# Optimization experiments

Hardware: AMD Instinct MI355X
Metric: run time of the kernel (lower is better)

Reference implementation:

```python
import jax, jax.numpy as jnp
import numpy as np

EPS = 1e-5

def conv2d(x, w, padding):
    # x: (N, Cin, H, W), w: (Cout, Cin, kh, kw)
    return jax.lax.conv_general_dilated(
        x, w, window_strides=(1, 1),
        padding=[(padding, padding), (padding, padding)],
        dimension_numbers=('NCHW', 'OIHW', 'NCHW'))

def proj_bn_relu(x, w, gamma, beta, mean, var):
    # 1x1 conv + BatchNorm (eval mode, running stats) + ReLU
    y = conv2d(x, w, 0)
    scale = (gamma / jnp.sqrt(var + EPS))[None, :, None, None]
    shift = (beta - mean * gamma / jnp.sqrt(var + EPS))[None, :, None, None]
    return jax.nn.relu(y * scale + shift)

def setup_inputs() -> dict:
    key = jax.random.key(0)
    ks = jax.random.split(key, 16)
    B, Sx, Sy, C1, C2, Co, H, W, K = 2, 4, 4, 64, 64, 64, 128, 128, 3
    inp = {
        'u': jax.random.normal(ks[0], (B, Sx, C1, H, W), jnp.float32),
        'v': jax.random.normal(ks[1], (B, Sy, C2, H, W), jnp.float32),
        'pu_w': jax.random.normal(ks[2], (C1, C1, 1, 1), jnp.float32) * 0.05,
        'pu_gamma': jnp.ones((C1,), jnp.float32),
        'pu_beta': jnp.zeros((C1,), jnp.float32),
        'pu_mean': jax.random.normal(ks[3], (C1,), jnp.float32) * 0.1,
        'pu_var': jax.random.uniform(ks[4], (C1,), jnp.float32, 0.5, 1.5),
        'pv_w': jax.random.normal(ks[5], (C2, C2, 1, 1), jnp.float32) * 0.05,
        'pv_gamma': jnp.ones((C2,), jnp.float32),
        'pv_beta': jnp.zeros((C2,), jnp.float32),
        'pv_mean': jax.random.normal(ks[6], (C2,), jnp.float32) * 0.1,
        'pv_var': jax.random.uniform(ks[7], (C2,), jnp.float32, 0.5, 1.5),
        'conv_w': jax.random.normal(ks[8], (Co, C1 + C2, K, K), jnp.float32) * 0.02,
        'conv_b': jax.random.normal(ks[9], (Co,), jnp.float32) * 0.02,
    }
    return inp

def reference(u, v, pu_w, pu_gamma, pu_beta, pu_mean, pu_var,
              pv_w, pv_gamma, pv_beta, pv_mean, pv_var, conv_w, conv_b):
    B, Sx, C1, H, W = u.shape
    _, Sy, C2, _, _ = v.shape
    pad = 1
    # flatten set dims into batch for the 1x1 proj+BN+ReLU
    uf = proj_bn_relu(u.reshape(B * Sx, C1, H, W), pu_w, pu_gamma, pu_beta, pu_mean, pu_var)
    vf = proj_bn_relu(v.reshape(B * Sy, C2, H, W), pv_w, pv_gamma, pv_beta, pv_mean, pv_var)
    # conv over concat channels is linear -> split weight and broadcast-add,
    # exactly equal to conv(cat(repeat(u), repeat(v))) without materializing
    # the (B,Sx,Sy,C1+C2,H,W) tensor.
    w_u = conv_w[:, :C1]   # (Co, C1, K, K)
    w_v = conv_w[:, C1:]   # (Co, C2, K, K)
    ou = conv2d(uf, w_u, pad)  # (B*Sx, Co, Ho, Wo)
    ov = conv2d(vf, w_v, pad)  # (B*Sy, Co, Ho, Wo)
    Co, Ho, Wo = ou.shape[1], ou.shape[2], ou.shape[3]
    ou = ou.reshape(B, Sx, 1, Co, Ho, Wo)
    ov = ov.reshape(B, 1, Sy, Co, Ho, Wo)
    out = ou + ov + conv_b[None, None, None, :, None, None]
    return out  # (B, Sx, Sy, Co, Ho, Wo)
```

## Files before the change

kernel.cpp:

```cpp
#include <hip/hip_runtime.h>
#include <hip/hip_bf16.h>

#define C   64
#define Hh  128
#define Ww  128
#define HW  16384

typedef __attribute__((ext_vector_type(8))) short bf16x8;
typedef __attribute__((ext_vector_type(4))) float f32x4;

__device__ __forceinline__ unsigned short f2bf(float f) {
    unsigned u = __builtin_bit_cast(unsigned, f);
    unsigned r = (u + 0x7fff + ((u >> 16) & 1)) >> 16;
    return (unsigned short)r;
}

__global__ __launch_bounds__(256) void prep_kernel(
    const float* __restrict__ pu_w, const float* __restrict__ pu_g,
    const float* __restrict__ pu_b, const float* __restrict__ pu_m,
    const float* __restrict__ pu_v,
    const float* __restrict__ pv_w, const float* __restrict__ pv_g,
    const float* __restrict__ pv_b, const float* __restrict__ pv_m,
    const float* __restrict__ pv_v,
    const float* __restrict__ conv_w,
    short* __restrict__ pwu, short* __restrict__ pwv,
    short* __restrict__ wpu, short* __restrict__ wpv,
    float* __restrict__ shu, float* __restrict__ shv)
{
    const int idx = blockIdx.x * 256 + threadIdx.x;
    if (idx < 8192) {
        const int c  = idx >> 12;
        const int r  = idx & 4095;
        const int co = r >> 6, ci = r & 63;
        const float* w = c ? pv_w : pu_w;
        const float* g = c ? pv_g : pu_g;
        const float* vv = c ? pv_v : pu_v;
        const float scale = g[co] * rsqrtf(vv[co] + 1e-5f);
        (c ? pwv : pwu)[r] = (short)f2bf(w[co * 64 + ci] * scale);
    } else if (idx < 81920) {
        const int flat = idx - 8192;
        const int c  = flat / 36864;
        const int r  = flat % 36864;
        const int ch  = r / 18432;
        const int r2  = r % 18432;
        const int tap = r2 / 2048;
        const int r3  = r2 & 2047;
        const int co = r3 >> 5, ci = r3 & 31;
        const float src = conv_w[(size_t)(co * 128 + c * 64 + ch * 32 + ci) * 9 + tap];
        (c ? wpv : wpu)[((ch * 9 + tap) * 64 + co) * 32 + ci] = (short)f2bf(src);
    } else if (idx < 82048) {
        const int r  = idx - 81920;
        const int c  = r >> 6, co = r & 63;
        const float* g = c ? pv_g : pu_g;
        const float* b = c ? pv_b : pu_b;
        const float* m = c ? pv_m : pu_m;
        const float* vv = c ? pv_v : pu_v;
        const float scale = g[co] * rsqrtf(vv[co] + 1e-5f);
        (c ? shv : shu)[co] = b[co] - m[co] * scale;
    }
}

__global__ __launch_bounds__(256) void proj_mfma(
    const float* __restrict__ x, const short* __restrict__ pw,
    const float* __restrict__ shiftg, short* __restrict__ y)
{
    __shared__ short xs[256 * 72];
    __shared__ short pwl[64 * 72];
    __shared__ float ssh[64];

    const int img  = blockIdx.y;
    const int pix0 = blockIdx.x * 256;
    const int tid  = threadIdx.x;

    const float* xi = x + (size_t)img * C * HW + pix0 + tid;
#pragma unroll 8
    for (int c2 = 0; c2 < 32; ++c2) {
        const float a = xi[(size_t)(2 * c2) * HW];
        const float b = xi[(size_t)(2 * c2 + 1) * HW];
        const int packed = (int)f2bf(a) | ((int)f2bf(b) << 16);
        *(int*)(&xs[tid * 72 + c2 * 2]) = packed;
    }
#pragma unroll
    for (int it = 0; it < 2; ++it) {
        const int idx = tid + it * 256;
        const int oct = idx & 7, co = idx >> 3;
        *(int4*)(&pwl[co * 72 + oct * 8]) = *(const int4*)(&pw[co * 64 + oct * 8]);
    }
    if (tid < 64) ssh[tid] = shiftg[tid];
    __syncthreads();

    const int wq = tid >> 6;
    const int lane = tid & 63;
    const int lx = lane & 15;
    const int q  = lane >> 4;

    f32x4 acc[4][4];
#pragma unroll
    for (int mt = 0; mt < 4; ++mt)
#pragma unroll
        for (int nt = 0; nt < 4; ++nt) acc[mt][nt] = (f32x4){0.f, 0.f, 0.f, 0.f};

#pragma unroll
    for (int kc = 0; kc < 2; ++kc) {
        bf16x8 a[4], b[4];
#pragma unroll
        for (int mt = 0; mt < 4; ++mt)
            a[mt] = *(const bf16x8*)&xs[((wq * 4 + mt) * 16 + lx) * 72 + kc * 32 + q * 8];
#pragma unroll
        for (int nt = 0; nt < 4; ++nt)
            b[nt] = *(const bf16x8*)&pwl[(nt * 16 + lx) * 72 + kc * 32 + q * 8];
#pragma unroll
        for (int mt = 0; mt < 4; ++mt)
#pragma unroll
            for (int nt = 0; nt < 4; ++nt)
                acc[mt][nt] = __builtin_amdgcn_mfma_f32_16x16x32_bf16(a[mt], b[nt], acc[mt][nt], 0, 0, 0);
    }

    short* yo = y + ((size_t)img * HW + pix0) * C;
#pragma unroll
    for (int mt = 0; mt < 4; ++mt)
#pragma unroll
        for (int nt = 0; nt < 4; ++nt)
#pragma unroll
            for (int r = 0; r < 4; ++r) {
                const int pixl = (wq * 4 + mt) * 16 + q * 4 + r;
                const int co = nt * 16 + lx;
                float vv = acc[mt][nt][r] + ssh[co];
                vv = fmaxf(vv, 0.f);
                yo[(size_t)pixl * C + co] = (short)f2bf(vv);
            }
}

__global__ __launch_bounds__(256, 2) void conv_mfma(
    const short* __restrict__ uf, const short* __restrict__ wp,
    float* __restrict__ out)
{
    __shared__ short xs[340 * 40];
    __shared__ short wsm[5 * 64 * 40];

    const int img = blockIdx.y;
    const int tx = blockIdx.x & 3, ty = blockIdx.x >> 2;
    const int h0 = ty * 8, w0 = tx * 32;
    const int tid = threadIdx.x;
    const int wq = tid >> 6;
    const int lane = tid & 63;
    const int lx = lane & 15;
    const int q8 = (lane >> 4) * 8;

    f32x4 acc[4][4];
#pragma unroll
    for (int mt = 0; mt < 4; ++mt)
#pragma unroll
        for (int nt = 0; nt < 4; ++nt) acc[mt][nt] = (f32x4){0.f, 0.f, 0.f, 0.f};

    const short* ub = uf + (size_t)img * HW * C;

    for (int ch = 0; ch < 2; ++ch) {
        __syncthreads();
        for (int idx = tid; idx < 1360; idx += 256) {
            const int oct = idx & 3;
            const int pcell = idx >> 2;
            const int h = pcell / 34, w = pcell - h * 34;
            const int gh = h0 - 1 + h, gw = w0 - 1 + w;
            int4 v = {0, 0, 0, 0};
            if (gh >= 0 && gh < Hh && gw >= 0 && gw < Ww)
                v = *(const int4*)&ub[(size_t)(gh * Ww + gw) * C + ch * 32 + oct * 8];
            *(int4*)(&xs[pcell * 40 + oct * 8]) = v;
        }
        for (int tg = 0; tg < 2; ++tg) {
            const int tb = tg ? 5 : 0;
            const int ntap = tg ? 4 : 5;
            if (tg) __syncthreads();
            for (int idx = tid; idx < ntap * 256; idx += 256) {
                const int oct = idx & 3;
                const int co = (idx >> 2) & 63;
                const int tl = idx >> 8;
                *(int4*)(&wsm[(tl * 64 + co) * 40 + oct * 8]) =
                    *(const int4*)&wp[(((ch * 9 + tb + tl) * 64) + co) * 32 + oct * 8];
            }
            __syncthreads();
            for (int tl = 0; tl < ntap; ++tl) {
                const int t = tb + tl;
                const int ky = (t < 3) ? 0 : ((t < 6) ? 1 : 2);
                const int kx = t - ky * 3;
                bf16x8 a[4], b[4];
#pragma unroll
                for (int mt = 0; mt < 4; ++mt)
                    a[mt] = *(const bf16x8*)&wsm[(tl * 64 + mt * 16 + lx) * 40 + q8];
#pragma unroll
                for (int nt = 0; nt < 4; ++nt) {
                    const int cell = (2 * wq + (nt >> 1) + ky) * 34 + (nt & 1) * 16 + lx + kx;
                    b[nt] = *(const bf16x8*)&xs[cell * 40 + q8];
                }
#pragma unroll
                for (int mt = 0; mt < 4; ++mt)
#pragma unroll
                    for (int nt = 0; nt < 4; ++nt)
                        acc[mt][nt] = __builtin_amdgcn_mfma_f32_16x16x32_bf16(a[mt], b[nt], acc[mt][nt], 0, 0, 0);
            }
        }
    }

    const int qq = lane >> 4;
    float* ob = out + (size_t)img * C * HW;
#pragma unroll
    for (int mt = 0; mt < 4; ++mt)
#pragma unroll
        for (int nt = 0; nt < 4; ++nt)
#pragma unroll
            for (int r = 0; r < 4; ++r) {
                const int co = mt * 16 + qq * 4 + r;
                const int h = h0 + 2 * wq + (nt >> 1);
                const int w = w0 + (nt & 1) * 16 + lx;
                ob[(size_t)co * HW + h * Ww + w] = acc[mt][nt][r];
            }
}

__global__ __launch_bounds__(256) void addb_kernel(
    const float* __restrict__ ou, const float* __restrict__ ov,
    const float* __restrict__ bias, float* __restrict__ out)
{
    const size_t i4 = (size_t)blockIdx.x * 256 + threadIdx.x;
    const int    hw4 = (int)(i4 & 4095);
    const size_t q   = i4 >> 12;
    const int co = (int)(q & 63);
    const size_t p = q >> 6;
    const int sy = (int)(p & 3);
    const int sx = (int)((p >> 2) & 3);
    const int b  = (int)(p >> 4);

    const float4 o1 = ((const float4*)ou)[((size_t)(b * 4 + sx) * C + co) * 4096 + hw4];
    const float4 o2 = ((const float4*)ov)[((size_t)(b * 4 + sy) * C + co) * 4096 + hw4];
    const float bb = bias[co];
    float4 r;
    r.x = o1.x + o2.x + bb;
    r.y = o1.y + o2.y + bb;
    r.z = o1.z + o2.z + bb;
    r.w = o1.w + o2.w + bb;
    ((float4*)out)[i4] = r;
}

extern "C" void kernel_launch(void* const* d_in, const int* in_sizes, int n_in,
                              void* d_out, int out_size, void* d_ws, size_t ws_size,
                              hipStream_t stream)
{
    const float* u        = (const float*)d_in[0];
    const float* v        = (const float*)d_in[1];
    const float* pu_w     = (const float*)d_in[2];
    const float* pu_gamma = (const float*)d_in[3];
    const float* pu_beta  = (const float*)d_in[4];
    const float* pu_mean  = (const float*)d_in[5];
    const float* pu_var   = (const float*)d_in[6];
    const float* pv_w     = (const float*)d_in[7];
    const float* pv_gamma = (const float*)d_in[8];
    const float* pv_beta  = (const float*)d_in[9];
    const float* pv_mean  = (const float*)d_in[10];
    const float* pv_var   = (const float*)d_in[11];
    const float* conv_w   = (const float*)d_in[12];
    const float* conv_b   = (const float*)d_in[13];
    float* out = (float*)d_out;

    char* ws = (char*)d_ws;
    short* uf  = (short*)(ws);
    short* vf  = (short*)(ws + 16777216);
    float* ou  = (float*)(ws + 33554432);
    float* ov  = (float*)(ws + 67108864);
    char*  aux = ws + 100663296;
    short* pwu = (short*)(aux);
    short* pwv = (short*)(aux + 8192);
    short* wpu = (short*)(aux + 16384);
    short* wpv = (short*)(aux + 90112);
    float* shu = (float*)(aux + 163840);
    float* shv = (float*)(aux + 164096);

    prep_kernel<<<321, 256, 0, stream>>>(pu_w, pu_gamma, pu_beta, pu_mean, pu_var,
                                         pv_w, pv_gamma, pv_beta, pv_mean, pv_var,
                                         conv_w, pwu, pwv, wpu, wpv, shu, shv);

    dim3 gp(64, 8);
    proj_mfma<<<gp, 256, 0, stream>>>(u, pwu, shu, uf);
    proj_mfma<<<gp, 256, 0, stream>>>(v, pwv, shv, vf);

    dim3 gc(64, 8);
    conv_mfma<<<gc, 256, 0, stream>>>(uf, wpu, ou);
    conv_mfma<<<gc, 256, 0, stream>>>(vf, wpv, ov);

    const size_t n4 = (size_t)out_size / 4;
    addb_kernel<<<(unsigned)(n4 / 256), 256, 0, stream>>>(ou, ov, conv_b, out);
}
```

Measured before the change: 279.8 us.

## Fuse 1x1 projection into 3x3 conv kernel and store conv outputs as bf16

Merges the projection+BN+ReLU step into the conv kernel. Each block converts the fp32 input tile plus its halo to bf16 in LDS, runs the 1x1 projection with MFMA in place, then runs the 3x3 conv from the same LDS tile. This removes the intermediate bf16 feature-map round trip and two launches, and u and v are handled in one launch via blockIdx.z. The conv partial outputs are now written as bf16 rather than fp32, halving their traffic into the broadcast-add kernel, which now reads 8 bf16 values per thread. In exchange, halo pixels are projected redundantly and the intermediate conv results lose precision.

```diff
diff --git a/kernel.cpp b/kernel.cpp
--- a/kernel.cpp
+++ b/kernel.cpp
@@ -13,6 +13,10 @@
     unsigned u = __builtin_bit_cast(unsigned, f);
     unsigned r = (u + 0x7fff + ((u >> 16) & 1)) >> 16;
     return (unsigned short)r;
+}
+__device__ __forceinline__ float bf2f(unsigned short h) {
+    unsigned u = ((unsigned)h) << 16;
+    return __builtin_bit_cast(float, u);
 }
 
 __global__ __launch_bounds__(256) void prep_kernel(
@@ -31,11 +35,12 @@
     if (idx < 8192) {
         const int c  = idx >> 12;
         const int r  = idx & 4095;
-        const int co = r >> 6, ci = r & 63;
+        const int co = r >> 6;
         const float* w = c ? pv_w : pu_w;
         const float* g = c ? pv_g : pu_g;
         const float* vv = c ? pv_v : pu_v;
         const float scale = g[co] * rsqrtf(vv[co] + 1e-5f);
+        const int ci = r & 63;
         (c ? pwv : pwu)[r] = (short)f2bf(w[co * 64 + ci] * scale);
     } else if (idx < 81920) {
         const int flat = idx - 8192;
@@ -60,92 +65,94 @@
     }
 }
 
-__global__ __launch_bounds__(256) void proj_mfma(
-    const float* __restrict__ x, const short* __restrict__ pw,
-    const float* __restrict__ shiftg, short* __restrict__ y)
-{
-    __shared__ short xs[256 * 72];
-    __shared__ short pwl[64 * 72];
+__global__ __launch_bounds__(256, 2) void fused_kernel(
+    const float* __restrict__ ug, const float* __restrict__ vg,
+    const short* __restrict__ pwu, const short* __restrict__ pwv,
+    const float* __restrict__ shu, const float* __restrict__ shv,
+    const short* __restrict__ wpu, const short* __restrict__ wpv,
+    short* __restrict__ oug, short* __restrict__ ovg)
+{
+    __shared__ short xs[352 * 72];
+    __shared__ short wbuf[3 * 64 * 40];
     __shared__ float ssh[64];
 
+    const int isv = blockIdx.z;
+    const float* x  = isv ? vg  : ug;
+    const short* pw = isv ? pwv : pwu;
+    const float* sh = isv ? shv : shu;
+    const short* wp = isv ? wpv : wpu;
+    short*       ot = isv ? ovg : oug;
+
     const int img  = blockIdx.y;
-    const int pix0 = blockIdx.x * 256;
-    const int tid  = threadIdx.x;
-
-    const float* xi = x + (size_t)img * C * HW + pix0 + tid;
-#pragma unroll 8
-    for (int c2 = 0; c2 < 32; ++c2) {
-        const float a = xi[(size_t)(2 * c2) * HW];
-        const float b = xi[(size_t)(2 * c2 + 1) * HW];
-        const int packed = (int)f2bf(a) | ((int)f2bf(b) << 16);
-        *(int*)(&xs[tid * 72 + c2 * 2]) = packed;
-    }
-#pragma unroll
-    for (int it = 0; it < 2; ++it) {
-        const int idx = tid + it * 256;
-        const int oct = idx & 7, co = idx >> 3;
-        *(int4*)(&pwl[co * 72 + oct * 8]) = *(const int4*)(&pw[co * 64 + oct * 8]);
-    }
-    if (tid < 64) ssh[tid] = shiftg[tid];
-    __syncthreads();
-
-    const int wq = tid >> 6;
-    const int lane = tid & 63;
-    const int lx = lane & 15;
-    const int q  = lane >> 4;
-
-    f32x4 acc[4][4];
-#pragma unroll
-    for (int mt = 0; mt < 4; ++mt)
-#pragma unroll
-        for (int nt = 0; nt < 4; ++nt) acc[mt][nt] = (f32x4){0.f, 0.f, 0.f, 0.f};
-
-#pragma unroll
-    for (int kc = 0; kc < 2; ++kc) {
-        bf16x8 a[4], b[4];
-#pragma unroll
-        for (int mt = 0; mt < 4; ++mt)
-            a[mt] = *(const bf16x8*)&xs[((wq * 4 + mt) * 16 + lx) * 72 + kc * 32 + q * 8];
-#pragma unroll
-        for (int nt = 0; nt < 4; ++nt)
-            b[nt] = *(const bf16x8*)&pwl[(nt * 16 + lx) * 72 + kc * 32 + q * 8];
-#pragma unroll
-        for (int mt = 0; mt < 4; ++mt)
-#pragma unroll
-            for (int nt = 0; nt < 4; ++nt)
-                acc[mt][nt] = __builtin_amdgcn_mfma_f32_16x16x32_bf16(a[mt], b[nt], acc[mt][nt], 0, 0, 0);
-    }
-
-    short* yo = y + ((size_t)img * HW + pix0) * C;
-#pragma unroll
-    for (int mt = 0; mt < 4; ++mt)
-#pragma unroll
-        for (int nt = 0; nt < 4; ++nt)
-#pragma unroll
-            for (int r = 0; r < 4; ++r) {
-                const int pixl = (wq * 4 + mt) * 16 + q * 4 + r;
-                const int co = nt * 16 + lx;
-                float vv = acc[mt][nt][r] + ssh[co];
-                vv = fmaxf(vv, 0.f);
-                yo[(size_t)pixl * C + co] = (short)f2bf(vv);
-            }
-}
-
-__global__ __launch_bounds__(256, 2) void conv_mfma(
-    const short* __restrict__ uf, const short* __restrict__ wp,
-    float* __restrict__ out)
-{
-    __shared__ short xs[340 * 40];
-    __shared__ short wsm[5 * 64 * 40];
-
-    const int img = blockIdx.y;
-    const int tx = blockIdx.x & 3, ty = blockIdx.x >> 2;
+    const int tile = blockIdx.x;
+    const int tx = tile & 3, ty = tile >> 2;
     const int h0 = ty * 8, w0 = tx * 32;
     const int tid = threadIdx.x;
     const int wq = tid >> 6;
     const int lane = tid & 63;
     const int lx = lane & 15;
-    const int q8 = (lane >> 4) * 8;
+    const int q  = lane >> 4;
+    const int q8 = q * 8;
+
+    const float* xi = x + (size_t)img * C * HW;
+    for (int it = 0; it < 43; ++it) {
+        const int idx = it * 256 + tid;
+        if (idx < 10880) {
+            const int p    = idx / 340;
+            const int cell = idx - p * 340;
+            const int r = cell / 34, cc = cell - r * 34;
+            const int gh = h0 - 1 + r, gw = w0 - 1 + cc;
+            int pk = 0;
+            if (gh >= 0 && gh < Hh && gw >= 0 && gw < Ww) {
+                const float a = xi[(size_t)(2 * p) * HW + gh * Ww + gw];
+                const float b = xi[(size_t)(2 * p + 1) * HW + gh * Ww + gw];
+                pk = (int)f2bf(a) | ((int)f2bf(b) << 16);
+            }
+            *(int*)&xs[cell * 72 + 2 * p] = pk;
+        }
+    }
+#pragma unroll
+    for (int itr = 0; itr < 2; ++itr) {
+        const int idx = itr * 256 + tid;
+        const int oct = idx & 7, co = idx >> 3;
+        *(int4*)&wbuf[co * 72 + oct * 8] = *(const int4*)&pw[co * 64 + oct * 8];
+    }
+    if (tid < 64) ssh[tid] = sh[tid];
+    __syncthreads();
+
+    {
+        bf16x8 bw[4][2];
+#pragma unroll
+        for (int nt = 0; nt < 4; ++nt)
+#pragma unroll
+            for (int kc = 0; kc < 2; ++kc)
+                bw[nt][kc] = *(const bf16x8*)&wbuf[(nt * 16 + lx) * 72 + kc * 32 + q8];
+
+        for (int mt = wq; mt < 22; mt += 4) {
+            const bf16x8 a0 = *(const bf16x8*)&xs[(mt * 16 + lx) * 72 + q8];
+            const bf16x8 a1 = *(const bf16x8*)&xs[(mt * 16 + lx) * 72 + 32 + q8];
+            f32x4 pa[4];
+#pragma unroll
+            for (int nt = 0; nt < 4; ++nt) {
+                pa[nt] = (f32x4){0.f, 0.f, 0.f, 0.f};
+                pa[nt] = __builtin_amdgcn_mfma_f32_16x16x32_bf16(a0, bw[nt][0], pa[nt], 0, 0, 0);
+                pa[nt] = __builtin_amdgcn_mfma_f32_16x16x32_bf16(a1, bw[nt][1], pa[nt], 0, 0, 0);
+            }
+#pragma unroll
+            for (int r = 0; r < 4; ++r) {
+                const int cell = mt * 16 + q * 4 + r;
+                const int rr = cell / 34, cc = cell - rr * 34;
+                const int gh = h0 - 1 + rr, gw = w0 - 1 + cc;
+                const bool inb = (cell < 340) & (gh >= 0) & (gh < Hh) & (gw >= 0) & (gw < Ww);
+#pragma unroll
+                for (int nt = 0; nt < 4; ++nt) {
+                    const float vv = fmaxf(pa[nt][r] + ssh[nt * 16 + lx], 0.f);
+                    xs[cell * 72 + nt * 16 + lx] = inb ? (short)f2bf(vv) : (short)0;
+                }
+            }
+        }
+    }
+    __syncthreads();
 
     f32x4 acc[4][4];
 #pragma unroll
@@ -153,44 +160,29 @@
 #pragma unroll
         for (int nt = 0; nt < 4; ++nt) acc[mt][nt] = (f32x4){0.f, 0.f, 0.f, 0.f};
 
-    const short* ub = uf + (size_t)img * HW * C;
-
     for (int ch = 0; ch < 2; ++ch) {
-        __syncthreads();
-        for (int idx = tid; idx < 1360; idx += 256) {
-            const int oct = idx & 3;
-            const int pcell = idx >> 2;
-            const int h = pcell / 34, w = pcell - h * 34;
-            const int gh = h0 - 1 + h, gw = w0 - 1 + w;
-            int4 v = {0, 0, 0, 0};
-            if (gh >= 0 && gh < Hh && gw >= 0 && gw < Ww)
-                v = *(const int4*)&ub[(size_t)(gh * Ww + gw) * C + ch * 32 + oct * 8];
-            *(int4*)(&xs[pcell * 40 + oct * 8]) = v;
-        }
-        for (int tg = 0; tg < 2; ++tg) {
-            const int tb = tg ? 5 : 0;
-            const int ntap = tg ? 4 : 5;
-            if (tg) __syncthreads();
-            for (int idx = tid; idx < ntap * 256; idx += 256) {
+        for (int ky = 0; ky < 3; ++ky) {
+            __syncthreads();
+#pragma unroll
+            for (int itr = 0; itr < 3; ++itr) {
+                const int idx = itr * 256 + tid;
                 const int oct = idx & 3;
-                const int co = (idx >> 2) & 63;
-                const int tl = idx >> 8;
-                *(int4*)(&wsm[(tl * 64 + co) * 40 + oct * 8]) =
-                    *(const int4*)&wp[(((ch * 9 + tb + tl) * 64) + co) * 32 + oct * 8];
+                const int co  = (idx >> 2) & 63;
+                const int tl  = idx >> 8;
+                *(int4*)&wbuf[(tl * 64 + co) * 40 + oct * 8] =
+                    *(const int4*)&wp[(((ch * 9 + ky * 3 + tl) * 64) + co) * 32 + oct * 8];
             }
             __syncthreads();
-            for (int tl = 0; tl < ntap; ++tl) {
-                const int t = tb + tl;
-                const int ky = (t < 3) ? 0 : ((t < 6) ? 1 : 2);
-                const int kx = t - ky * 3;
+#pragma unroll
+            for (int kx = 0; kx < 3; ++kx) {
                 bf16x8 a[4], b[4];
 #pragma unroll
                 for (int mt = 0; mt < 4; ++mt)
-                    a[mt] = *(const bf16x8*)&wsm[(tl * 64 + mt * 16 + lx) * 40 + q8];
+                    a[mt] = *(const bf16x8*)&wbuf[(kx * 64 + mt * 16 + lx) * 40 + q8];
 #pragma unroll
                 for (int nt = 0; nt < 4; ++nt) {
                     const int cell = (2 * wq + (nt >> 1) + ky) * 34 + (nt & 1) * 16 + lx + kx;
-                    b[nt] = *(const bf16x8*)&xs[cell * 40 + q8];
+                    b[nt] = *(const bf16x8*)&xs[cell * 72 + ch * 32 + q8];
                 }
 #pragma unroll
                 for (int mt = 0; mt < 4; ++mt)
@@ -201,43 +193,48 @@
         }
     }
 
-    const int qq = lane >> 4;
-    float* ob = out + (size_t)img * C * HW;
+    short* ob = ot + (size_t)img * C * HW;
 #pragma unroll
     for (int mt = 0; mt < 4; ++mt)
 #pragma unroll
         for (int nt = 0; nt < 4; ++nt)
 #pragma unroll
             for (int r = 0; r < 4; ++r) {
-                const int co = mt * 16 + qq * 4 + r;
+                const int co = mt * 16 + q * 4 + r;
                 const int h = h0 + 2 * wq + (nt >> 1);
                 const int w = w0 + (nt & 1) * 16 + lx;
-                ob[(size_t)co * HW + h * Ww + w] = acc[mt][nt][r];
+                ob[(size_t)co * HW + h * Ww + w] = (short)f2bf(acc[mt][nt][r]);
             }
 }
 
 __global__ __launch_bounds__(256) void addb_kernel(
-    const float* __restrict__ ou, const float* __restrict__ ov,
+    const unsigned short* __restrict__ ou, const unsigned short* __restrict__ ov,
     const float* __restrict__ bias, float* __restrict__ out)
 {
-    const size_t i4 = (size_t)blockIdx.x * 256 + threadIdx.x;
-    const int    hw4 = (int)(i4 & 4095);
-    const size_t q   = i4 >> 12;
-    const int co = (int)(q & 63);
-    const size_t p = q >> 6;
+    const size_t i8 = (size_t)blockIdx.x * 256 + threadIdx.x;
+    const int    hw8 = (int)(i8 & 2047);
+    const size_t qq  = i8 >> 11;
+    const int co = (int)(qq & 63);
+    const size_t p = qq >> 6;
     const int sy = (int)(p & 3);
     const int sx = (int)((p >> 2) & 3);
     const int b  = (int)(p >> 4);
 
-    const float4 o1 = ((const float4*)ou)[((size_t)(b * 4 + sx) * C + co) * 4096 + hw4];
-    const float4 o2 = ((const float4*)ov)[((size_t)(b * 4 + sy) * C + co) * 4096 + hw4];
+    const int4 lu = *(const int4*)&ou[((size_t)(b * 4 + sx) * C + co) * HW + hw8 * 8];
+    const int4 lv = *(const int4*)&ov[((size_t)(b * 4 + sy) * C + co) * HW + hw8 * 8];
     const float bb = bias[co];
-    float4 r;
-    r.x = o1.x + o2.x + bb;
-    r.y = o1.y + o2.y + bb;
-    r.z = o1.z + o2.z + bb;
-    r.w = o1.w + o2.w + bb;
-    ((float4*)out)[i4] = r;
+
+    float r[8];
+    const int uu[4] = {lu.x, lu.y, lu.z, lu.w};
+    const int vv[4] = {lv.x, lv.y, lv.z, lv.w};
+#pragma unroll
+    for (int k = 0; k < 4; ++k) {
+        r[2 * k]     = bf2f((unsigned short)(uu[k] & 0xffff)) + bf2f((unsigned short)(vv[k] & 0xffff)) + bb;
+        r[2 * k + 1] = bf2f((unsigned short)((unsigned)uu[k] >> 16)) + bf2f((unsigned short)((unsigned)vv[k] >> 16)) + bb;
+    }
+    float4* o = (float4*)(out + i8 * 8);
+    o[0] = (float4){r[0], r[1], r[2], r[3]};
+    o[1] = (float4){r[4], r[5], r[6], r[7]};
 }
 
 extern "C" void kernel_launch(void* const* d_in, const int* in_sizes, int n_in,
@@ -261,11 +258,9 @@
     float* out = (float*)d_out;
 
     char* ws = (char*)d_ws;
-    short* uf  = (short*)(ws);
-    short* vf  = (short*)(ws + 16777216);
-    float* ou  = (float*)(ws + 33554432);
-    float* ov  = (float*)(ws + 67108864);
-    char*  aux = ws + 100663296;
+    short* ou  = (short*)(ws);
+    short* ov  = (short*)(ws + 16777216);
+    char*  aux = ws + 33554432;
     short* pwu = (short*)(aux);
     short* pwv = (short*)(aux + 8192);
     short* wpu = (short*)(aux + 16384);
@@ -277,14 +272,9 @@
                                          pv_w, pv_gamma, pv_beta, pv_mean, pv_var,
                                          conv_w, pwu, pwv, wpu, wpv, shu, shv);
 
-    dim3 gp(64, 8);
-    proj_mfma<<<gp, 256, 0, stream>>>(u, pwu, shu, uf);
-    proj_mfma<<<gp, 256, 0, stream>>>(v, pwv, shv, vf);
-
-    dim3 gc(64, 8);
-    conv_mfma<<<gc, 256, 0, stream>>>(uf, wpu, ou);
-    conv_mfma<<<gc, 256, 0, stream>>>(vf, wpv, ov);
-
-    const size_t n4 = (size_t)out_size / 4;
-    addb_kernel<<<(unsigned)(n4 / 256), 256, 0, stream>>>(ou, ov, conv_b, out);
-}
+    dim3 gf(64, 8, 2);
+    fused_kernel<<<gf, 256, 0, stream>>>(u, v, pwu, pwv, shu, shv, wpu, wpv, ou, ov);
+
+    addb_kernel<<<16384, 256, 0, stream>>>((const unsigned short*)ou,
+                                           (const unsigned short*)ov, conv_b, out);
+}
```

Measured after the change: 309.6 us. 10.7% more time.
